# Performance work log

Measured on AMD Instinct MI355X. Metric: run time of the kernel, lower is better.

## Reference

```python
import jax, jax.numpy as jnp
import numpy as np
import math

D_MODEL = 2048
K = 64
W = 512              # window_size
STRIDE = W // 2      # = 256
EMA_ALPHA = 0.9
N_RETRIEVE = 8
EPS = 1e-12


def _build_cheby(k, w):
    # cheby_mat[k, n] = cos(k * arccos(t_n)), t_n = cos(pi*(2n+1)/(2w))
    ns = np.arange(w, dtype=np.float64)
    t = np.cos(np.pi * (2 * ns + 1) / (2 * w))
    ks = np.arange(k, dtype=np.float64)
    return jnp.asarray(np.cos(ks[:, None] * np.arccos(t)[None, :]), dtype=jnp.float32)


def setup_inputs() -> dict:
    key = jax.random.key(0)
    ks = jax.random.split(key, 5)
    B, S = 2, 8192
    scan_out = jax.random.normal(ks[0], (B, S, D_MODEL), dtype=jnp.float32)
    buf = jax.random.normal(ks[1], (W, D_MODEL), dtype=jnp.float32)  # pre-filled circular buffer
    # unit-modulus random-phase complex roles: r_k[d] = exp(i*theta)
    phases = jax.random.uniform(ks[2], (K, D_MODEL), dtype=jnp.float32) * (2.0 * math.pi)
    roles_real = jnp.cos(phases)
    roles_imag = jnp.sin(phases)
    w_bands = 1.0 / (jnp.arange(K, dtype=jnp.float32) + 1.0)  # w_init = 1/(k+1)
    retrieve_proj_w = jax.random.normal(ks[3], (D_MODEL, D_MODEL), dtype=jnp.float32) * 0.02
    inject_gate = jnp.zeros((1,), dtype=jnp.float32)
    cheby_mat = _build_cheby(K, W)
    return dict(scan_out=scan_out, buf=buf, roles_real=roles_real, roles_imag=roles_imag,
                w_bands=w_bands, retrieve_proj_w=retrieve_proj_w, inject_gate=inject_gate,
                cheby_mat=cheby_mat)


def reference(scan_out, buf, roles_real, roles_imag, w_bands, retrieve_proj_w, inject_gate, cheby_mat):
    S = scan_out.shape[1]
    h_mean = scan_out.mean(axis=0)                      # [S, D] batch-mean like torch code
    n_chunks = S // STRIDE
    chunks = h_mean.reshape(n_chunks, STRIDE, D_MODEL)  # each chunk triggers one bind

    init = (buf, jnp.int32(0),
            jnp.zeros((K, D_MODEL), jnp.float32),   # c_past
            jnp.zeros((D_MODEL,), jnp.float32),     # V_mem_real
            jnp.zeros((D_MODEL,), jnp.float32),     # V_mem_imag
            jnp.zeros((K,), jnp.float32),           # _coeff_norms (EMA)
            jnp.zeros((K,), jnp.float32))           # spectral_delta

    def step(carry, chunk):
        b, pos, c_past, vr, vi, cnorms, _ = carry
        # circular-buffer write of `stride` tokens starting at pos
        b = jax.lax.dynamic_update_slice(b, chunk, (pos, 0))
        pos = (pos + STRIDE) % W
        order = (jnp.arange(W, dtype=jnp.int32) + pos) % W   # oldest-first reorder
        data = b[order]                                      # [W, D]
        # Chebyshev coefficients: c = (2/W) * cheby_mat @ data, c0 halved
        coeffs = (2.0 / W) * (cheby_mat @ data)              # [K, D]
        coeffs = coeffs.at[0].multiply(0.5)
        # HRR-normalized bind into holographic memory via EMA
        norms = jnp.maximum(jnp.linalg.norm(coeffs, axis=-1, keepdims=True), EPS)
        cn = coeffs / norms
        cnorms = EMA_ALPHA * cnorms + (1.0 - EMA_ALPHA) * norms[:, 0]
        vr = EMA_ALPHA * vr + (1.0 - EMA_ALPHA) * (cn * roles_real).sum(axis=0)
        vi = EMA_ALPHA * vi + (1.0 - EMA_ALPHA) * (cn * roles_imag).sum(axis=0)
        # spectral delta vs previous window's coefficients
        delta = jnp.linalg.norm(coeffs - c_past, axis=-1)    # [K]
        return (b, pos, coeffs, vr, vi, cnorms, delta), None

    (b, pos, c_now, vr, vi, cnorms, delta), _ = jax.lax.scan(step, init, chunks)

    # retrieve: unbind top-J bands by spectral delta, denormalize, weight, project
    _, top = jax.lax.top_k(delta, N_RETRIEVE)                # [J]
    rr = roles_real[top]
    ri = roles_imag[top]
    retrieved = (vr[None, :] * rr + vi[None, :] * ri) * jnp.maximum(cnorms[top], EPS)[:, None]  # [J, D]
    weights = jax.nn.softplus(w_bands[top])                  # [J]
    ctx = (weights[:, None] * retrieved).sum(axis=0)         # [D]
    out = (ctx @ retrieve_proj_w.T) * jax.nn.sigmoid(inject_gate[0])  # [D]
    return out, delta, vr, vi
```

## Files before the change

kernel.cpp:

```cpp
#include <hip/hip_runtime.h>
#include <math.h>

#define D_MODEL 2048
#define KB_ 64
#define NCHUNK 32

typedef __bf16 bf16;
typedef __attribute__((ext_vector_type(8))) __bf16 bf16x8;
typedef __attribute__((ext_vector_type(4))) __bf16 bf16x4;
typedef __attribute__((ext_vector_type(4))) float f32x4;

#define OFF_COEFFS 0
#define OFF_NSQ    (32 * 64 * 2048)
#define OFF_NORMS  (OFF_NSQ + 32 * 64 * 32)
#define OFF_VR     (OFF_NORMS + 2048)
#define OFF_VI     (OFF_VR + 2048)
#define OFF_CTX    (OFF_VI + 2048)
#define OFF_CHEB2  (OFF_CTX + 2048)
#define OFF_HM     (OFF_CHEB2 + 16384)

__global__ __launch_bounds__(256) void k0_prep(
    const float* __restrict__ scan, const float* __restrict__ cheby,
    bf16* __restrict__ hm, bf16* __restrict__ cheb2, float* __restrict__ vzero)
{
  const int b = blockIdx.x;
  const int t = threadIdx.x;
  if (b < 8192) {
    const float* p0 = scan + b * 2048 + t * 8;
    const float* p1 = p0 + 8192 * 2048;
    float4 a0 = *(const float4*)(p0);
    float4 a1 = *(const float4*)(p0 + 4);
    float4 b0 = *(const float4*)(p1);
    float4 b1 = *(const float4*)(p1 + 4);
    bf16x8 e = {(bf16)(0.5f * (a0.x + b0.x)), (bf16)(0.5f * (a0.y + b0.y)),
                (bf16)(0.5f * (a0.z + b0.z)), (bf16)(0.5f * (a0.w + b0.w)),
                (bf16)(0.5f * (a1.x + b1.x)), (bf16)(0.5f * (a1.y + b1.y)),
                (bf16)(0.5f * (a1.z + b1.z)), (bf16)(0.5f * (a1.w + b1.w))};
    *(bf16x8*)(hm + b * 2048 + t * 8) = e;
  } else if (b < 8208) {
    int idx = (b - 8192) * 2048 + t * 8;
    float4 c0 = *(const float4*)(cheby + idx);
    float4 c1 = *(const float4*)(cheby + idx + 4);
    bf16x8 e = {(bf16)c0.x, (bf16)c0.y, (bf16)c0.z, (bf16)c0.w,
                (bf16)c1.x, (bf16)c1.y, (bf16)c1.z, (bf16)c1.w};
    *(bf16x8*)(cheb2 + idx) = e;
  } else {
    float4 z = make_float4(0.f, 0.f, 0.f, 0.f);
#pragma unroll
    for (int i = 0; i < 4; ++i)
      *(float4*)(vzero + t * 16 + i * 4) = z;
  }
}

__global__ __launch_bounds__(256) void k1_mfma(
    const bf16* __restrict__ hm, const float* __restrict__ buf,
    const bf16* __restrict__ cheb2, float* __restrict__ coeffs,
    float* __restrict__ nsq_part)
{
  __shared__ bf16 Bs[64 * 72];

  const int t = threadIdx.x;
  const int dt = blockIdx.x;
  const int c  = blockIdx.y;
  const int w = t >> 6, lane = t & 63;
  const int quad = lane >> 4, r16 = lane & 15;
  const int d0 = dt * 64;
  const int n0 = (t >> 4) * 4;
  const int d4 = (t & 15) * 4;

  f32x4 acc[4];
#pragma unroll
  for (int tn = 0; tn < 4; ++tn) acc[tn] = (f32x4){0.f, 0.f, 0.f, 0.f};

  for (int nb = 0; nb < 8; ++nb) {
    const bf16* abase = cheb2 + (w * 16 + r16) * 512 + nb * 64 + quad * 8;
    bf16x8 a0 = *(const bf16x8*)(abase);
    bf16x8 a1 = *(const bf16x8*)(abase + 32);

    bf16x4 rowv[4];
    if (c == 0 && nb < 4) {
      const float* bp = buf + (256 + nb * 64 + n0) * 2048 + d0 + d4;
#pragma unroll
      for (int i = 0; i < 4; ++i) {
        float4 v = *(const float4*)(bp + i * 2048);
        rowv[i] = (bf16x4){(bf16)v.x, (bf16)v.y, (bf16)v.z, (bf16)v.w};
      }
    } else {
      const bf16* hp = hm + (c * 256 - 256 + nb * 64 + n0) * 2048 + d0 + d4;
#pragma unroll
      for (int i = 0; i < 4; ++i)
        rowv[i] = *(const bf16x4*)(hp + i * 2048);
    }
    __syncthreads();
#pragma unroll
    for (int x = 0; x < 4; ++x) {
      bf16x4 e = {rowv[0][x], rowv[1][x], rowv[2][x], rowv[3][x]};
      *(bf16x4*)(Bs + (d4 + x) * 72 + n0) = e;
    }
    __syncthreads();

#pragma unroll
    for (int ks = 0; ks < 2; ++ks) {
      bf16x8 a = ks ? a1 : a0;
#pragma unroll
      for (int tn = 0; tn < 4; ++tn) {
        bf16x8 bfr = *(const bf16x8*)(Bs + (tn * 16 + r16) * 72 + ks * 32 + quad * 8);
        acc[tn] = __builtin_amdgcn_mfma_f32_16x16x32_bf16(a, bfr, acc[tn], 0, 0, 0);
      }
    }
  }

  const float scale = 2.0f / 512.0f;
  float sq[4] = {0.f, 0.f, 0.f, 0.f};
#pragma unroll
  for (int tn = 0; tn < 4; ++tn) {
#pragma unroll
    for (int rr = 0; rr < 4; ++rr) {
      int band = w * 16 + quad * 4 + rr;
      float sc = (band == 0) ? scale * 0.5f : scale;
      float v = acc[tn][rr] * sc;
      coeffs[(c * 64 + band) * 2048 + d0 + tn * 16 + r16] = v;
      sq[rr] += v * v;
    }
  }
#pragma unroll
  for (int off = 8; off > 0; off >>= 1) {
#pragma unroll
    for (int rr = 0; rr < 4; ++rr) sq[rr] += __shfl_down(sq[rr], off);
  }
  if (r16 == 0) {
#pragma unroll
    for (int rr = 0; rr < 4; ++rr)
      nsq_part[(c * 64 + w * 16 + quad * 4 + rr) * 32 + dt] = sq[rr];
  }
}

__global__ __launch_bounds__(256) void kd_delta(
    const float* __restrict__ coeffs, float* __restrict__ dout)
{
  const int k = blockIdx.x, tid = threadIdx.x;
  const float* p1 = coeffs + (31 * 64 + k) * 2048;
  const float* p0 = coeffs + (30 * 64 + k) * 2048;
  float s = 0.f;
#pragma unroll
  for (int i = 0; i < 2; ++i) {
    float4 a = *(const float4*)(p1 + tid * 4 + i * 1024);
    float4 b = *(const float4*)(p0 + tid * 4 + i * 1024);
    float x = a.x - b.x, y = a.y - b.y, z = a.z - b.z, ww = a.w - b.w;
    s += x * x + y * y + z * z + ww * ww;
  }
  for (int o = 32; o > 0; o >>= 1) s += __shfl_down(s, o, 64);
  __shared__ float red[4];
  if ((tid & 63) == 0) red[tid >> 6] = s;
  __syncthreads();
  if (tid == 0) dout[D_MODEL + k] = sqrtf(red[0] + red[1] + red[2] + red[3]);
}

__global__ __launch_bounds__(256) void k3_bind(
    const float* __restrict__ coeffs, const float* __restrict__ nsq_part,
    const float* __restrict__ rr, const float* __restrict__ ri,
    float* __restrict__ vr, float* __restrict__ vi,
    float* __restrict__ norms)
{
  __shared__ float inv_s[64];
  const int tid = threadIdx.x;
  const int c = blockIdx.y;
  if (tid < 64) {
    float s = 0.f;
#pragma unroll
    for (int dt = 0; dt < 32; ++dt) s += nsq_part[(c * 64 + tid) * 32 + dt];
    float nrm = fmaxf(sqrtf(s), 1e-12f);
    inv_s[tid] = 1.0f / nrm;
    if (blockIdx.x == 0) norms[c * 64 + tid] = nrm;
  }
  __syncthreads();
  const int d = blockIdx.x * 256 + tid;
  const float wc = 0.1f * powf(0.9f, (float)(31 - c));
  float ar = 0.f, ai = 0.f;
#pragma unroll 8
  for (int k = 0; k < KB_; ++k) {
    float cf = coeffs[(c * 64 + k) * 2048 + d] * inv_s[k];
    ar += cf * rr[k * D_MODEL + d];
    ai += cf * ri[k * D_MODEL + d];
  }
  atomicAdd(&vr[d], wc * ar);
  atomicAdd(&vi[d], wc * ai);
}

__global__ __launch_bounds__(256) void k4_ctx(
    const float* __restrict__ norms, const float* __restrict__ vr,
    const float* __restrict__ vi, const float* __restrict__ rr,
    const float* __restrict__ ri, const float* __restrict__ wbands,
    float* __restrict__ dout, float* __restrict__ ctx)
{
  __shared__ float cn_s[64];
  __shared__ int top_s[8];
  __shared__ float wgt_s[8];
  const int tid = threadIdx.x;
  const int d = blockIdx.x * 256 + tid;
  if (tid < 64) {
    float s = 0.f;
    for (int c = 0; c < NCHUNK; ++c) s = 0.9f * s + 0.1f * norms[c * 64 + tid];
    cn_s[tid] = fmaxf(s, 1e-12f);
  }
  __syncthreads();
  if (tid == 0) {
    unsigned long long taken = 0ULL;
    for (int jj = 0; jj < 8; ++jj) {
      float best = -1.f;
      int bi = 0;
      for (int k = 0; k < 64; ++k) {
        float dv = dout[D_MODEL + k];
        if (!((taken >> k) & 1ULL) && dv > best) { best = dv; bi = k; }
      }
      taken |= (1ULL << bi);
      top_s[jj] = bi;
      wgt_s[jj] = log1pf(expf(wbands[bi]));
    }
  }
  __syncthreads();
  float sr = vr[d];
  float si = vi[d];
  dout[D_MODEL + KB_ + d] = sr;
  dout[D_MODEL + KB_ + D_MODEL + d] = si;
  float cx = 0.f;
#pragma unroll
  for (int jj = 0; jj < 8; ++jj) {
    int k = top_s[jj];
    cx += wgt_s[jj] * (sr * rr[k * D_MODEL + d] + si * ri[k * D_MODEL + d]) * cn_s[k];
  }
  ctx[d] = cx;
}

__global__ __launch_bounds__(256) void k5b_gemv(
    const float* __restrict__ Wp, const float* __restrict__ ctx,
    const float* __restrict__ gate, float* __restrict__ dout)
{
  const int tid = threadIdx.x;
  const int lane = tid & 63;
  const int w = tid >> 6;
  const int row = blockIdx.x * 4 + w;
  const float* p = Wp + row * D_MODEL;
  float s = 0.f;
#pragma unroll
  for (int i = 0; i < 8; ++i) {
    int e = lane * 4 + i * 256;
    float4 wv = *(const float4*)(p + e);
    float4 cv = *(const float4*)(ctx + e);
    s += wv.x * cv.x + wv.y * cv.y + wv.z * cv.z + wv.w * cv.w;
  }
  for (int o = 32; o > 0; o >>= 1) s += __shfl_down(s, o, 64);
  if (lane == 0) {
    float sig = 1.f / (1.f + expf(-gate[0]));
    dout[row] = s * sig;
  }
}

extern "C" void kernel_launch(void* const* d_in, const int* in_sizes, int n_in,
                              void* d_out, int out_size, void* d_ws, size_t ws_size,
                              hipStream_t stream) {
  const float* scan  = (const float*)d_in[0];
  const float* buf   = (const float*)d_in[1];
  const float* rr    = (const float*)d_in[2];
  const float* ri    = (const float*)d_in[3];
  const float* wb    = (const float*)d_in[4];
  const float* Wp    = (const float*)d_in[5];
  const float* gate  = (const float*)d_in[6];
  const float* cheby = (const float*)d_in[7];
  float* out = (float*)d_out;
  float* ws = (float*)d_ws;

  float* coeffs   = ws + OFF_COEFFS;
  float* nsq_part = ws + OFF_NSQ;
  float* norms    = ws + OFF_NORMS;
  float* vr       = ws + OFF_VR;
  float* vi       = ws + OFF_VI;
  float* ctx      = ws + OFF_CTX;
  bf16*  cheb2    = (bf16*)(ws + OFF_CHEB2);
  bf16*  hm       = (bf16*)(ws + OFF_HM);

  k0_prep<<<8209, 256, 0, stream>>>(scan, cheby, hm, cheb2, vr);
  k1_mfma<<<dim3(32, 32), 256, 0, stream>>>(hm, buf, cheb2, coeffs, nsq_part);
  kd_delta<<<64, 256, 0, stream>>>(coeffs, out);
  k3_bind<<<dim3(8, NCHUNK), 256, 0, stream>>>(coeffs, nsq_part, rr, ri,
                                               vr, vi, norms);
  k4_ctx<<<8, 256, 0, stream>>>(norms, vr, vi, rr, ri, wb, out, ctx);
  k5b_gemv<<<512, 256, 0, stream>>>(Wp, ctx, gate, out);
}
```

Before: 278.0 us.

## Fuse all stages into one cooperative persistent kernel with grid syncs

Replaces the six separate launches with a single cooperative kernel. The stages loop over work units with a grid stride and are separated by grid-wide barriers. The spectral-delta reduction moves into the bind stage for the last chunk and accumulates squared differences with atomics. The bind stage is split into 16-band groups, which gives more parallel work units. The aim is to remove launch overhead and the separate delta pass, at the cost of grid-sync latency and a grid capped at 1024 blocks for the bandwidth-heavy prep phase.

```diff
diff --git a/kernel.cpp b/kernel.cpp
--- a/kernel.cpp
+++ b/kernel.cpp
@@ -1,5 +1,8 @@
 #include <hip/hip_runtime.h>
+#include <hip/hip_cooperative_groups.h>
 #include <math.h>
+
+namespace cg = cooperative_groups;
 
 #define D_MODEL 2048
 #define KB_ 64
@@ -15,244 +18,247 @@
 #define OFF_NORMS  (OFF_NSQ + 32 * 64 * 32)
 #define OFF_VR     (OFF_NORMS + 2048)
 #define OFF_VI     (OFF_VR + 2048)
-#define OFF_CTX    (OFF_VI + 2048)
+#define OFF_DSQ    (OFF_VI + 2048)
+#define OFF_CTX    (OFF_DSQ + 64)
 #define OFF_CHEB2  (OFF_CTX + 2048)
 #define OFF_HM     (OFF_CHEB2 + 16384)
 
-__global__ __launch_bounds__(256) void k0_prep(
-    const float* __restrict__ scan, const float* __restrict__ cheby,
-    bf16* __restrict__ hm, bf16* __restrict__ cheb2, float* __restrict__ vzero)
+__global__ __launch_bounds__(256, 4) void mega(
+    const float* __restrict__ scan, const float* __restrict__ buf,
+    const float* __restrict__ rr, const float* __restrict__ ri,
+    const float* __restrict__ wb, const float* __restrict__ Wp,
+    const float* __restrict__ gate, const float* __restrict__ cheby,
+    float* __restrict__ dout, float* __restrict__ ws)
 {
+  cg::grid_group gg = cg::this_grid();
+  const int G = gridDim.x;
   const int b = blockIdx.x;
   const int t = threadIdx.x;
-  if (b < 8192) {
-    const float* p0 = scan + b * 2048 + t * 8;
-    const float* p1 = p0 + 8192 * 2048;
-    float4 a0 = *(const float4*)(p0);
-    float4 a1 = *(const float4*)(p0 + 4);
-    float4 b0 = *(const float4*)(p1);
-    float4 b1 = *(const float4*)(p1 + 4);
-    bf16x8 e = {(bf16)(0.5f * (a0.x + b0.x)), (bf16)(0.5f * (a0.y + b0.y)),
-                (bf16)(0.5f * (a0.z + b0.z)), (bf16)(0.5f * (a0.w + b0.w)),
-                (bf16)(0.5f * (a1.x + b1.x)), (bf16)(0.5f * (a1.y + b1.y)),
-                (bf16)(0.5f * (a1.z + b1.z)), (bf16)(0.5f * (a1.w + b1.w))};
-    *(bf16x8*)(hm + b * 2048 + t * 8) = e;
-  } else if (b < 8208) {
-    int idx = (b - 8192) * 2048 + t * 8;
-    float4 c0 = *(const float4*)(cheby + idx);
-    float4 c1 = *(const float4*)(cheby + idx + 4);
-    bf16x8 e = {(bf16)c0.x, (bf16)c0.y, (bf16)c0.z, (bf16)c0.w,
-                (bf16)c1.x, (bf16)c1.y, (bf16)c1.z, (bf16)c1.w};
-    *(bf16x8*)(cheb2 + idx) = e;
-  } else {
-    float4 z = make_float4(0.f, 0.f, 0.f, 0.f);
-#pragma unroll
-    for (int i = 0; i < 4; ++i)
-      *(float4*)(vzero + t * 16 + i * 4) = z;
-  }
-}
-
-__global__ __launch_bounds__(256) void k1_mfma(
-    const bf16* __restrict__ hm, const float* __restrict__ buf,
-    const bf16* __restrict__ cheb2, float* __restrict__ coeffs,
-    float* __restrict__ nsq_part)
-{
-  __shared__ bf16 Bs[64 * 72];
-
-  const int t = threadIdx.x;
-  const int dt = blockIdx.x;
-  const int c  = blockIdx.y;
-  const int w = t >> 6, lane = t & 63;
-  const int quad = lane >> 4, r16 = lane & 15;
-  const int d0 = dt * 64;
-  const int n0 = (t >> 4) * 4;
-  const int d4 = (t & 15) * 4;
-
-  f32x4 acc[4];
-#pragma unroll
-  for (int tn = 0; tn < 4; ++tn) acc[tn] = (f32x4){0.f, 0.f, 0.f, 0.f};
-
-  for (int nb = 0; nb < 8; ++nb) {
-    const bf16* abase = cheb2 + (w * 16 + r16) * 512 + nb * 64 + quad * 8;
-    bf16x8 a0 = *(const bf16x8*)(abase);
-    bf16x8 a1 = *(const bf16x8*)(abase + 32);
-
-    bf16x4 rowv[4];
-    if (c == 0 && nb < 4) {
-      const float* bp = buf + (256 + nb * 64 + n0) * 2048 + d0 + d4;
-#pragma unroll
-      for (int i = 0; i < 4; ++i) {
-        float4 v = *(const float4*)(bp + i * 2048);
-        rowv[i] = (bf16x4){(bf16)v.x, (bf16)v.y, (bf16)v.z, (bf16)v.w};
-      }
+  const int lane = t & 63;
+
+  float* coeffs = ws + OFF_COEFFS;
+  float* nsq    = ws + OFF_NSQ;
+  float* norms  = ws + OFF_NORMS;
+  float* vr     = ws + OFF_VR;
+  float* vi     = ws + OFF_VI;
+  float* dsq    = ws + OFF_DSQ;
+  float* ctx    = ws + OFF_CTX;
+  bf16*  cheb2  = (bf16*)(ws + OFF_CHEB2);
+  bf16*  hm     = (bf16*)(ws + OFF_HM);
+
+  __shared__ __align__(16) char smem_raw[64 * 72 * 2];
+
+  for (int u = b; u < 8209; u += G) {
+    if (u < 8192) {
+      const float* p0 = scan + u * 2048 + t * 8;
+      const float* p1 = p0 + 8192 * 2048;
+      float4 a0 = *(const float4*)(p0);
+      float4 a1 = *(const float4*)(p0 + 4);
+      float4 b0 = *(const float4*)(p1);
+      float4 b1 = *(const float4*)(p1 + 4);
+      bf16x8 e = {(bf16)(0.5f * (a0.x + b0.x)), (bf16)(0.5f * (a0.y + b0.y)),
+                  (bf16)(0.5f * (a0.z + b0.z)), (bf16)(0.5f * (a0.w + b0.w)),
+                  (bf16)(0.5f * (a1.x + b1.x)), (bf16)(0.5f * (a1.y + b1.y)),
+                  (bf16)(0.5f * (a1.z + b1.z)), (bf16)(0.5f * (a1.w + b1.w))};
+      *(bf16x8*)(hm + u * 2048 + t * 8) = e;
+    } else if (u < 8208) {
+      int idx = (u - 8192) * 2048 + t * 8;
+      float4 c0 = *(const float4*)(cheby + idx);
+      float4 c1 = *(const float4*)(cheby + idx + 4);
+      bf16x8 e = {(bf16)c0.x, (bf16)c0.y, (bf16)c0.z, (bf16)c0.w,
+                  (bf16)c1.x, (bf16)c1.y, (bf16)c1.z, (bf16)c1.w};
+      *(bf16x8*)(cheb2 + idx) = e;
     } else {
-      const bf16* hp = hm + (c * 256 - 256 + nb * 64 + n0) * 2048 + d0 + d4;
-#pragma unroll
-      for (int i = 0; i < 4; ++i)
-        rowv[i] = *(const bf16x4*)(hp + i * 2048);
-    }
-    __syncthreads();
-#pragma unroll
-    for (int x = 0; x < 4; ++x) {
-      bf16x4 e = {rowv[0][x], rowv[1][x], rowv[2][x], rowv[3][x]};
-      *(bf16x4*)(Bs + (d4 + x) * 72 + n0) = e;
-    }
-    __syncthreads();
-
-#pragma unroll
-    for (int ks = 0; ks < 2; ++ks) {
-      bf16x8 a = ks ? a1 : a0;
+      for (int i = t; i < 4160; i += 256) vr[i] = 0.f;
+    }
+  }
+  gg.sync();
+
+  {
+    bf16* Bs = (bf16*)smem_raw;
+    const int w    = t >> 6;
+    const int quad = lane >> 4, r16 = lane & 15;
+    const int n0 = (t >> 4) * 4;
+    const int d4 = (t & 15) * 4;
+
+    for (int u = b; u < 1024; u += G) {
+      const int dt = u & 31, c = u >> 5;
+      const int d0 = dt * 64;
+
+      f32x4 acc[4];
+#pragma unroll
+      for (int tn = 0; tn < 4; ++tn) acc[tn] = (f32x4){0.f, 0.f, 0.f, 0.f};
+
+      for (int nb = 0; nb < 8; ++nb) {
+        const bf16* abase = cheb2 + (w * 16 + r16) * 512 + nb * 64 + quad * 8;
+        bf16x8 a0 = *(const bf16x8*)(abase);
+        bf16x8 a1 = *(const bf16x8*)(abase + 32);
+
+        bf16x4 rowv[4];
+        if (c == 0 && nb < 4) {
+          const float* bp = buf + (256 + nb * 64 + n0) * 2048 + d0 + d4;
+#pragma unroll
+          for (int i = 0; i < 4; ++i) {
+            float4 v = *(const float4*)(bp + i * 2048);
+            rowv[i] = (bf16x4){(bf16)v.x, (bf16)v.y, (bf16)v.z, (bf16)v.w};
+          }
+        } else {
+          const bf16* hp = hm + (c * 256 - 256 + nb * 64 + n0) * 2048 + d0 + d4;
+#pragma unroll
+          for (int i = 0; i < 4; ++i)
+            rowv[i] = *(const bf16x4*)(hp + i * 2048);
+        }
+        __syncthreads();
+#pragma unroll
+        for (int x = 0; x < 4; ++x) {
+          bf16x4 e = {rowv[0][x], rowv[1][x], rowv[2][x], rowv[3][x]};
+          *(bf16x4*)(Bs + (d4 + x) * 72 + n0) = e;
+        }
+        __syncthreads();
+
+#pragma unroll
+        for (int ks = 0; ks < 2; ++ks) {
+          bf16x8 a = ks ? a1 : a0;
+#pragma unroll
+          for (int tn = 0; tn < 4; ++tn) {
+            bf16x8 bfr = *(const bf16x8*)(Bs + (tn * 16 + r16) * 72 + ks * 32 + quad * 8);
+            acc[tn] = __builtin_amdgcn_mfma_f32_16x16x32_bf16(a, bfr, acc[tn], 0, 0, 0);
+          }
+        }
+      }
+
+      const float scale = 2.0f / 512.0f;
+      float sq[4] = {0.f, 0.f, 0.f, 0.f};
 #pragma unroll
       for (int tn = 0; tn < 4; ++tn) {
-        bf16x8 bfr = *(const bf16x8*)(Bs + (tn * 16 + r16) * 72 + ks * 32 + quad * 8);
-        acc[tn] = __builtin_amdgcn_mfma_f32_16x16x32_bf16(a, bfr, acc[tn], 0, 0, 0);
-      }
-    }
-  }
-
-  const float scale = 2.0f / 512.0f;
-  float sq[4] = {0.f, 0.f, 0.f, 0.f};
-#pragma unroll
-  for (int tn = 0; tn < 4; ++tn) {
-#pragma unroll
-    for (int rr = 0; rr < 4; ++rr) {
-      int band = w * 16 + quad * 4 + rr;
-      float sc = (band == 0) ? scale * 0.5f : scale;
-      float v = acc[tn][rr] * sc;
-      coeffs[(c * 64 + band) * 2048 + d0 + tn * 16 + r16] = v;
-      sq[rr] += v * v;
-    }
-  }
-#pragma unroll
-  for (int off = 8; off > 0; off >>= 1) {
-#pragma unroll
-    for (int rr = 0; rr < 4; ++rr) sq[rr] += __shfl_down(sq[rr], off);
-  }
-  if (r16 == 0) {
-#pragma unroll
-    for (int rr = 0; rr < 4; ++rr)
-      nsq_part[(c * 64 + w * 16 + quad * 4 + rr) * 32 + dt] = sq[rr];
-  }
-}
-
-__global__ __launch_bounds__(256) void kd_delta(
-    const float* __restrict__ coeffs, float* __restrict__ dout)
-{
-  const int k = blockIdx.x, tid = threadIdx.x;
-  const float* p1 = coeffs + (31 * 64 + k) * 2048;
-  const float* p0 = coeffs + (30 * 64 + k) * 2048;
-  float s = 0.f;
-#pragma unroll
-  for (int i = 0; i < 2; ++i) {
-    float4 a = *(const float4*)(p1 + tid * 4 + i * 1024);
-    float4 b = *(const float4*)(p0 + tid * 4 + i * 1024);
-    float x = a.x - b.x, y = a.y - b.y, z = a.z - b.z, ww = a.w - b.w;
-    s += x * x + y * y + z * z + ww * ww;
-  }
-  for (int o = 32; o > 0; o >>= 1) s += __shfl_down(s, o, 64);
-  __shared__ float red[4];
-  if ((tid & 63) == 0) red[tid >> 6] = s;
-  __syncthreads();
-  if (tid == 0) dout[D_MODEL + k] = sqrtf(red[0] + red[1] + red[2] + red[3]);
-}
-
-__global__ __launch_bounds__(256) void k3_bind(
-    const float* __restrict__ coeffs, const float* __restrict__ nsq_part,
-    const float* __restrict__ rr, const float* __restrict__ ri,
-    float* __restrict__ vr, float* __restrict__ vi,
-    float* __restrict__ norms)
-{
-  __shared__ float inv_s[64];
-  const int tid = threadIdx.x;
-  const int c = blockIdx.y;
-  if (tid < 64) {
+#pragma unroll
+        for (int rq = 0; rq < 4; ++rq) {
+          int band = w * 16 + quad * 4 + rq;
+          float sc = (band == 0) ? scale * 0.5f : scale;
+          float v = acc[tn][rq] * sc;
+          coeffs[(c * 64 + band) * 2048 + d0 + tn * 16 + r16] = v;
+          sq[rq] += v * v;
+        }
+      }
+#pragma unroll
+      for (int off = 8; off > 0; off >>= 1) {
+#pragma unroll
+        for (int rq = 0; rq < 4; ++rq) sq[rq] += __shfl_down(sq[rq], off);
+      }
+      if (r16 == 0) {
+#pragma unroll
+        for (int rq = 0; rq < 4; ++rq)
+          nsq[(c * 64 + w * 16 + quad * 4 + rq) * 32 + dt] = sq[rq];
+      }
+    }
+  }
+  gg.sync();
+
+  {
+    float* inv_s = (float*)smem_raw;
+    for (int u = b; u < 1024; u += G) {
+      const int c = u >> 5, s = u & 31;
+      const int kg = s >> 3, xi = s & 7;
+      __syncthreads();
+      if (t < 16) {
+        int k = kg * 16 + t;
+        float ssum = 0.f;
+#pragma unroll
+        for (int dtile = 0; dtile < 32; ++dtile) ssum += nsq[(c * 64 + k) * 32 + dtile];
+        float nrm = fmaxf(sqrtf(ssum), 1e-12f);
+        inv_s[t] = 1.0f / nrm;
+        if (xi == 0) norms[c * 64 + k] = nrm;
+      }
+      __syncthreads();
+      const int d = xi * 256 + t;
+      const float wc = 0.1f * powf(0.9f, (float)(31 - c));
+      float ar = 0.f, ai = 0.f;
+      if (c == 31) {
+        for (int kk = 0; kk < 16; ++kk) {
+          int k = kg * 16 + kk;
+          float cf = coeffs[(c * 64 + k) * 2048 + d];
+          float cn = cf * inv_s[kk];
+          ar += cn * rr[k * 2048 + d];
+          ai += cn * ri[k * 2048 + d];
+          float diff = cf - coeffs[(30 * 64 + k) * 2048 + d];
+          float sqv = diff * diff;
+#pragma unroll
+          for (int o = 32; o > 0; o >>= 1) sqv += __shfl_down(sqv, o, 64);
+          if (lane == 0) atomicAdd(&dsq[k], sqv);
+        }
+      } else {
+        for (int kk = 0; kk < 16; ++kk) {
+          int k = kg * 16 + kk;
+          float cn = coeffs[(c * 64 + k) * 2048 + d] * inv_s[kk];
+          ar += cn * rr[k * 2048 + d];
+          ai += cn * ri[k * 2048 + d];
+        }
+      }
+      atomicAdd(&vr[d], wc * ar);
+      atomicAdd(&vi[d], wc * ai);
+    }
+  }
+  gg.sync();
+
+  {
+    float* cn_s  = (float*)smem_raw;
+    int*   top_s = (int*)(smem_raw + 256);
+    float* wgt_s = (float*)(smem_raw + 288);
+    for (int u = b; u < 8; u += G) {
+      const int d = u * 256 + t;
+      __syncthreads();
+      if (t < 64) {
+        float s = 0.f;
+        for (int c = 0; c < NCHUNK; ++c) s = 0.9f * s + 0.1f * norms[c * 64 + t];
+        cn_s[t] = fmaxf(s, 1e-12f);
+      }
+      if (u == 0 && t < 64) dout[D_MODEL + t] = sqrtf(dsq[t]);
+      if (t == 0) {
+        unsigned long long taken = 0ULL;
+        for (int jj = 0; jj < 8; ++jj) {
+          float best = -1.f;
+          int bi = 0;
+          for (int k = 0; k < 64; ++k) {
+            float dv = sqrtf(dsq[k]);
+            if (!((taken >> k) & 1ULL) && dv > best) { best = dv; bi = k; }
+          }
+          taken |= (1ULL << bi);
+          top_s[jj] = bi;
+          wgt_s[jj] = log1pf(expf(wb[bi]));
+        }
+      }
+      __syncthreads();
+      float sr = vr[d], si = vi[d];
+      dout[D_MODEL + KB_ + d] = sr;
+      dout[D_MODEL + KB_ + D_MODEL + d] = si;
+      float cx = 0.f;
+#pragma unroll
+      for (int jj = 0; jj < 8; ++jj) {
+        int k = top_s[jj];
+        cx += wgt_s[jj] * (sr * rr[k * D_MODEL + d] + si * ri[k * D_MODEL + d]) * cn_s[k];
+      }
+      ctx[d] = cx;
+    }
+  }
+  gg.sync();
+
+  for (int u = b; u < 512; u += G) {
+    const int row = u * 4 + (t >> 6);
+    const float* p = Wp + row * D_MODEL;
     float s = 0.f;
 #pragma unroll
-    for (int dt = 0; dt < 32; ++dt) s += nsq_part[(c * 64 + tid) * 32 + dt];
-    float nrm = fmaxf(sqrtf(s), 1e-12f);
-    inv_s[tid] = 1.0f / nrm;
-    if (blockIdx.x == 0) norms[c * 64 + tid] = nrm;
-  }
-  __syncthreads();
-  const int d = blockIdx.x * 256 + tid;
-  const float wc = 0.1f * powf(0.9f, (float)(31 - c));
-  float ar = 0.f, ai = 0.f;
-#pragma unroll 8
-  for (int k = 0; k < KB_; ++k) {
-    float cf = coeffs[(c * 64 + k) * 2048 + d] * inv_s[k];
-    ar += cf * rr[k * D_MODEL + d];
-    ai += cf * ri[k * D_MODEL + d];
-  }
-  atomicAdd(&vr[d], wc * ar);
-  atomicAdd(&vi[d], wc * ai);
-}
-
-__global__ __launch_bounds__(256) void k4_ctx(
-    const float* __restrict__ norms, const float* __restrict__ vr,
-    const float* __restrict__ vi, const float* __restrict__ rr,
-    const float* __restrict__ ri, const float* __restrict__ wbands,
-    float* __restrict__ dout, float* __restrict__ ctx)
-{
-  __shared__ float cn_s[64];
-  __shared__ int top_s[8];
-  __shared__ float wgt_s[8];
-  const int tid = threadIdx.x;
-  const int d = blockIdx.x * 256 + tid;
-  if (tid < 64) {
-    float s = 0.f;
-    for (int c = 0; c < NCHUNK; ++c) s = 0.9f * s + 0.1f * norms[c * 64 + tid];
-    cn_s[tid] = fmaxf(s, 1e-12f);
-  }
-  __syncthreads();
-  if (tid == 0) {
-    unsigned long long taken = 0ULL;
-    for (int jj = 0; jj < 8; ++jj) {
-      float best = -1.f;
-      int bi = 0;
-      for (int k = 0; k < 64; ++k) {
-        float dv = dout[D_MODEL + k];
-        if (!((taken >> k) & 1ULL) && dv > best) { best = dv; bi = k; }
-      }
-      taken |= (1ULL << bi);
-      top_s[jj] = bi;
-      wgt_s[jj] = log1pf(expf(wbands[bi]));
-    }
-  }
-  __syncthreads();
-  float sr = vr[d];
-  float si = vi[d];
-  dout[D_MODEL + KB_ + d] = sr;
-  dout[D_MODEL + KB_ + D_MODEL + d] = si;
-  float cx = 0.f;
-#pragma unroll
-  for (int jj = 0; jj < 8; ++jj) {
-    int k = top_s[jj];
-    cx += wgt_s[jj] * (sr * rr[k * D_MODEL + d] + si * ri[k * D_MODEL + d]) * cn_s[k];
-  }
-  ctx[d] = cx;
-}
-
-__global__ __launch_bounds__(256) void k5b_gemv(
-    const float* __restrict__ Wp, const float* __restrict__ ctx,
-    const float* __restrict__ gate, float* __restrict__ dout)
-{
-  const int tid = threadIdx.x;
-  const int lane = tid & 63;
-  const int w = tid >> 6;
-  const int row = blockIdx.x * 4 + w;
-  const float* p = Wp + row * D_MODEL;
-  float s = 0.f;
-#pragma unroll
-  for (int i = 0; i < 8; ++i) {
-    int e = lane * 4 + i * 256;
-    float4 wv = *(const float4*)(p + e);
-    float4 cv = *(const float4*)(ctx + e);
-    s += wv.x * cv.x + wv.y * cv.y + wv.z * cv.z + wv.w * cv.w;
-  }
-  for (int o = 32; o > 0; o >>= 1) s += __shfl_down(s, o, 64);
-  if (lane == 0) {
-    float sig = 1.f / (1.f + expf(-gate[0]));
-    dout[row] = s * sig;
+    for (int i = 0; i < 8; ++i) {
+      int e = lane * 4 + i * 256;
+      float4 wv = *(const float4*)(p + e);
+      float4 cv = *(const float4*)(ctx + e);
+      s += wv.x * cv.x + wv.y * cv.y + wv.z * cv.z + wv.w * cv.w;
+    }
+#pragma unroll
+    for (int o = 32; o > 0; o >>= 1) s += __shfl_down(s, o, 64);
+    if (lane == 0) {
+      float sig = 1.f / (1.f + expf(-gate[0]));
+      dout[row] = s * sig;
+    }
   }
 }
 
@@ -270,20 +276,16 @@
   float* out = (float*)d_out;
   float* ws = (float*)d_ws;
 
-  float* coeffs   = ws + OFF_COEFFS;
-  float* nsq_part = ws + OFF_NSQ;
-  float* norms    = ws + OFF_NORMS;
-  float* vr       = ws + OFF_VR;
-  float* vi       = ws + OFF_VI;
-  float* ctx      = ws + OFF_CTX;
-  bf16*  cheb2    = (bf16*)(ws + OFF_CHEB2);
-  bf16*  hm       = (bf16*)(ws + OFF_HM);
-
-  k0_prep<<<8209, 256, 0, stream>>>(scan, cheby, hm, cheb2, vr);
-  k1_mfma<<<dim3(32, 32), 256, 0, stream>>>(hm, buf, cheb2, coeffs, nsq_part);
-  kd_delta<<<64, 256, 0, stream>>>(coeffs, out);
-  k3_bind<<<dim3(8, NCHUNK), 256, 0, stream>>>(coeffs, nsq_part, rr, ri,
-                                               vr, vi, norms);
-  k4_ctx<<<8, 256, 0, stream>>>(norms, vr, vi, rr, ri, wb, out, ctx);
-  k5b_gemv<<<512, 256, 0, stream>>>(Wp, ctx, gate, out);
+  static int gB = 0;
+  if (gB == 0) {
+    int nb = 0;
+    hipOccupancyMaxActiveBlocksPerMultiprocessor(&nb, (const void*)mega, 256, 0);
+    if (nb < 1) nb = 1;
+    gB = nb * 256;
+    if (gB > 1024) gB = 1024;
+  }
+
+  void* args[] = {(void*)&scan, (void*)&buf, (void*)&rr, (void*)&ri, (void*)&wb,
+                  (void*)&Wp, (void*)&gate, (void*)&cheby, (void*)&out, (void*)&ws};
+  hipLaunchCooperativeKernel((const void*)mega, dim3(gB), dim3(256), args, 0, stream);
 }
```

After: 553.1 us. +98.9%, slower.
